# Performance work log

Hardware: AMD Instinct MI355X
Metric: run time of the kernel (lower is better)

The kernel has to match this reference:

```python
import jax, jax.numpy as jnp
import numpy as np

N = 50000
E = 800000
D_IN = 128
D_OUT = 128
LN_EPS = 1e-5
DROP_P = 0.1


def setup_inputs() -> dict:
    key = jax.random.key(0)
    ks = jax.random.split(key, 8)
    x = jax.random.normal(ks[0], (N, D_IN), dtype=jnp.float32)
    edge_index = jax.random.randint(ks[1], (2, E), 0, N, dtype=jnp.int64)
    # dropout mask: binary keep-mask scaled by 1/(1-p), as torch dropout produces
    u = jax.random.uniform(ks[2], (N, D_IN), dtype=jnp.float32)
    dropout_mask = (u > DROP_P).astype(jnp.float32) / (1.0 - DROP_P)
    # LayerNorm affine params
    gamma = jnp.ones((D_IN,), dtype=jnp.float32)
    beta = jnp.zeros((D_IN,), dtype=jnp.float32)
    # SAGEConv linears: lin_l (aggregated neighbors, with bias), lin_r (root, no bias)
    s = 1.0 / np.sqrt(D_IN)
    w_l = jax.random.uniform(ks[3], (D_OUT, D_IN), minval=-s, maxval=s, dtype=jnp.float32)
    b_l = jax.random.uniform(ks[4], (D_OUT,), minval=-s, maxval=s, dtype=jnp.float32)
    w_r = jax.random.uniform(ks[5], (D_OUT, D_IN), minval=-s, maxval=s, dtype=jnp.float32)
    return {"x": x, "edge_index": edge_index, "dropout_mask": dropout_mask,
            "gamma": gamma, "beta": beta, "w_l": w_l, "b_l": b_l, "w_r": w_r}


def reference(x, edge_index, dropout_mask, gamma, beta, w_l, b_l, w_r):
    # LayerNorm + ReLU + dropout mask
    mu = jnp.mean(x, axis=-1, keepdims=True)
    var = jnp.mean(jnp.square(x - mu), axis=-1, keepdims=True)
    h = (x - mu) * jax.lax.rsqrt(var + LN_EPS) * gamma + beta
    h = jax.nn.relu(h) * dropout_mask  # [N, D_IN]
    # SAGEConv: mean-aggregate source features into target nodes
    src = edge_index[0]
    dst = edge_index[1]
    msg = h[src]  # [E, D_IN] gathered messages
    agg = jax.ops.segment_sum(msg, dst, num_segments=N)  # [N, D_IN]
    deg = jax.ops.segment_sum(jnp.ones((E,), dtype=h.dtype), dst, num_segments=N)
    agg = agg / jnp.maximum(deg, 1.0)[:, None]
    # out = lin_l(agg) + lin_r(h)
    out = agg @ w_l.T + b_l + h @ w_r.T  # [N, D_OUT]
    return out
```

## Files before the change

kernel.cpp:

```cpp
#include <hip/hip_runtime.h>
#include <hip/hip_bf16.h>

#define N_NODES 50000
#define N_EDGES 800000
#define D 128
#define NB_SCAN ((N_NODES + 255) / 256)

typedef short bf16x8 __attribute__((ext_vector_type(8)));
typedef float f32x4 __attribute__((ext_vector_type(4)));

__device__ __forceinline__ unsigned int bf16u(float f) {
  __hip_bfloat16 b = __float2bfloat16(f);
  return (unsigned int)*reinterpret_cast<unsigned short*>(&b);
}

__global__ __launch_bounds__(256) void gemm_kernel(
    const float* __restrict__ x, const float* __restrict__ mask,
    const float* __restrict__ gamma, const float* __restrict__ beta,
    const float* __restrict__ w_l, const float* __restrict__ w_r,
    const float* __restrict__ b_l, unsigned int* __restrict__ gb,
    float* __restrict__ rp, int* __restrict__ deg) {
  __shared__ unsigned short Bs[64 * 64 * 8];
  const int t = threadIdx.x;
  const int w = t >> 6;
  const int l = t & 63;
  const int lm = l & 15;
  const int quad = l >> 4;
  const int nb = blockIdx.x * 64;

  if (blockIdx.x < NB_SCAN) {
    const int i = blockIdx.x * 256 + t;
    if (i < N_NODES) deg[i] = 0;
  }

#pragma unroll
  for (int i = 0; i < 16; ++i) {
    const int fid = w * 16 + i;
    const int sub = fid >> 2;
    const int ch = fid & 3;
    const float* srcw = (sub < 8) ? (w_l + (size_t)(sub * 16 + lm) * D)
                                  : (w_r + (size_t)((sub - 8) * 16 + lm) * D);
    const float4 a = *(const float4*)(srcw + ch * 32 + quad * 8);
    const float4 b = *(const float4*)(srcw + ch * 32 + quad * 8 + 4);
    uint4 v;
    v.x = (bf16u(a.y) << 16) | bf16u(a.x);
    v.y = (bf16u(a.w) << 16) | bf16u(a.z);
    v.z = (bf16u(b.y) << 16) | bf16u(b.x);
    v.w = (bf16u(b.w) << 16) | bf16u(b.z);
    *(uint4*)(Bs + ((size_t)fid * 64 + l) * 8) = v;
  }

  int anode = nb + w * 16 + lm;
  if (anode >= N_NODES) anode = N_NODES - 1;
  const float* xrow = x + (size_t)anode * D;
  float xv[32];
  float s = 0.f, q = 0.f;
#pragma unroll
  for (int ch = 0; ch < 4; ++ch) {
    const float4 a = *(const float4*)(xrow + ch * 32 + quad * 8);
    const float4 b = *(const float4*)(xrow + ch * 32 + quad * 8 + 4);
    xv[ch * 8 + 0] = a.x; xv[ch * 8 + 1] = a.y;
    xv[ch * 8 + 2] = a.z; xv[ch * 8 + 3] = a.w;
    xv[ch * 8 + 4] = b.x; xv[ch * 8 + 5] = b.y;
    xv[ch * 8 + 6] = b.z; xv[ch * 8 + 7] = b.w;
    s += (a.x + a.y) + (a.z + a.w) + (b.x + b.y) + (b.z + b.w);
    q += a.x * a.x + a.y * a.y + a.z * a.z + a.w * a.w +
         b.x * b.x + b.y * b.y + b.z * b.z + b.w * b.w;
  }
  s += __shfl_xor(s, 16);
  s += __shfl_xor(s, 32);
  q += __shfl_xor(q, 16);
  q += __shfl_xor(q, 32);
  const float mean = s * (1.0f / 128.0f);
  const float var = q * (1.0f / 128.0f) - mean * mean;
  const float rs = rsqrtf(var + 1e-5f);

  const float* mrow = mask + (size_t)anode * D;
  bf16x8 af[4];
#pragma unroll
  for (int ch = 0; ch < 4; ++ch) {
    const int c0 = ch * 32 + quad * 8;
    const float4 g0 = *(const float4*)(gamma + c0);
    const float4 g1 = *(const float4*)(gamma + c0 + 4);
    const float4 b0 = *(const float4*)(beta + c0);
    const float4 b1 = *(const float4*)(beta + c0 + 4);
    const float4 m0 = *(const float4*)(mrow + c0);
    const float4 m1 = *(const float4*)(mrow + c0 + 4);
    const float gv[8] = {g0.x, g0.y, g0.z, g0.w, g1.x, g1.y, g1.z, g1.w};
    const float bv[8] = {b0.x, b0.y, b0.z, b0.w, b1.x, b1.y, b1.z, b1.w};
    const float mv[8] = {m0.x, m0.y, m0.z, m0.w, m1.x, m1.y, m1.z, m1.w};
#pragma unroll
    for (int j = 0; j < 8; ++j) {
      const float hv =
          fmaxf((xv[ch * 8 + j] - mean) * rs * gv[j] + bv[j], 0.0f) * mv[j];
      af[ch][j] = (short)bf16u(hv);
    }
  }
  __syncthreads();

  f32x4 acc[16];
#pragma unroll
  for (int sub = 0; sub < 16; ++sub) acc[sub] = (f32x4){0.f, 0.f, 0.f, 0.f};
  const bf16x8* BsF = (const bf16x8*)Bs;
#pragma unroll
  for (int sub = 0; sub < 16; ++sub)
#pragma unroll
    for (int ch = 0; ch < 4; ++ch)
      acc[sub] = __builtin_amdgcn_mfma_f32_16x16x32_bf16(
          af[ch], BsF[(sub * 4 + ch) * 64 + l], acc[sub], 0, 0, 0);

  float blv[8];
#pragma unroll
  for (int j = 0; j < 8; ++j) blv[j] = b_l[j * 16 + lm];

  const int node0 = nb + w * 16 + quad * 4;
#pragma unroll
  for (int reg = 0; reg < 4; ++reg) {
    const int node = node0 + reg;
    if (node < N_NODES) {
      uint4 p;
      p.x = (bf16u(acc[1][reg]) << 16) | bf16u(acc[0][reg]);
      p.y = (bf16u(acc[3][reg]) << 16) | bf16u(acc[2][reg]);
      p.z = (bf16u(acc[5][reg]) << 16) | bf16u(acc[4][reg]);
      p.w = (bf16u(acc[7][reg]) << 16) | bf16u(acc[6][reg]);
      ((uint4*)gb)[(size_t)node * 16 + lm] = p;
      float4 q0, q1;
      q0.x = acc[8][reg] + blv[0];
      q0.y = acc[9][reg] + blv[1];
      q0.z = acc[10][reg] + blv[2];
      q0.w = acc[11][reg] + blv[3];
      q1.x = acc[12][reg] + blv[4];
      q1.y = acc[13][reg] + blv[5];
      q1.z = acc[14][reg] + blv[6];
      q1.w = acc[15][reg] + blv[7];
      ((float4*)rp)[(size_t)node * 32 + lm * 2 + 0] = q0;
      ((float4*)rp)[(size_t)node * 32 + lm * 2 + 1] = q1;
    }
  }
}

__global__ __launch_bounds__(256) void hist_kernel(const int* __restrict__ ei,
                                                   int* __restrict__ deg,
                                                   int* __restrict__ rank) {
  const int e = (blockIdx.x * 256 + threadIdx.x) * 4;
  if (e + 3 < N_EDGES) {
    const int4 d4 = *(const int4*)(ei + N_EDGES + e);
    int4 r4;
    r4.x = atomicAdd(&deg[d4.x], 1);
    r4.y = atomicAdd(&deg[d4.y], 1);
    r4.z = atomicAdd(&deg[d4.z], 1);
    r4.w = atomicAdd(&deg[d4.w], 1);
    *(int4*)(rank + e) = r4;
  } else {
    for (int k = e; k < N_EDGES; ++k)
      rank[k] = atomicAdd(&deg[ei[N_EDGES + k]], 1);
  }
}

__global__ __launch_bounds__(256) void scan1_kernel(
    const int* __restrict__ deg, int* __restrict__ offL1,
    int* __restrict__ partial) {
  __shared__ int sm[256];
  const int t = threadIdx.x;
  const int i = blockIdx.x * 256 + t;
  const int v = (i < N_NODES) ? deg[i] : 0;
  sm[t] = v;
  __syncthreads();
#pragma unroll
  for (int ofs = 1; ofs < 256; ofs <<= 1) {
    int x = sm[t];
    if (t >= ofs) x += sm[t - ofs];
    __syncthreads();
    sm[t] = x;
    __syncthreads();
  }
  if (i < N_NODES) offL1[i] = sm[t] - v;
  if (t == 255) partial[blockIdx.x] = sm[255];
}

__global__ __launch_bounds__(256) void scan2_kernel(int* __restrict__ partial) {
  __shared__ int sm[256];
  const int t = threadIdx.x;
  const int v = (t < NB_SCAN) ? partial[t] : 0;
  sm[t] = v;
  __syncthreads();
#pragma unroll
  for (int ofs = 1; ofs < 256; ofs <<= 1) {
    int x = sm[t];
    if (t >= ofs) x += sm[t - ofs];
    __syncthreads();
    sm[t] = x;
    __syncthreads();
  }
  if (t < NB_SCAN) partial[t] = sm[t] - v;
}

__global__ __launch_bounds__(256) void scatter_kernel(
    const int* __restrict__ ei, const int* __restrict__ offL1,
    const int* __restrict__ partial, const int* __restrict__ rank,
    int* __restrict__ csr) {
  const int e = (blockIdx.x * 256 + threadIdx.x) * 4;
  if (e + 3 < N_EDGES) {
    const int4 s4 = *(const int4*)(ei + e);
    const int4 d4 = *(const int4*)(ei + N_EDGES + e);
    const int4 r4 = *(const int4*)(rank + e);
    csr[offL1[d4.x] + partial[d4.x >> 8] + r4.x] = s4.x;
    csr[offL1[d4.y] + partial[d4.y >> 8] + r4.y] = s4.y;
    csr[offL1[d4.z] + partial[d4.z >> 8] + r4.z] = s4.z;
    csr[offL1[d4.w] + partial[d4.w >> 8] + r4.w] = s4.w;
  } else {
    for (int k = e; k < N_EDGES; ++k) {
      const int dst = ei[N_EDGES + k];
      csr[offL1[dst] + partial[dst >> 8] + rank[k]] = ei[k];
    }
  }
}

#define ACC8(v)                                     \
  do {                                              \
    acc[0] += __uint_as_float((v).x << 16);         \
    acc[1] += __uint_as_float((v).x & 0xffff0000u); \
    acc[2] += __uint_as_float((v).y << 16);         \
    acc[3] += __uint_as_float((v).y & 0xffff0000u); \
    acc[4] += __uint_as_float((v).z << 16);         \
    acc[5] += __uint_as_float((v).z & 0xffff0000u); \
    acc[6] += __uint_as_float((v).w << 16);         \
    acc[7] += __uint_as_float((v).w & 0xffff0000u); \
  } while (0)

__global__ __launch_bounds__(256) void agg_kernel(
    const int* __restrict__ offL1, const int* __restrict__ partial,
    const int* __restrict__ csr, const unsigned int* __restrict__ gb,
    const float* __restrict__ rp, float* __restrict__ out) {
  const int l = threadIdx.x & 63;
  const int q = l >> 4;
  const int c = l & 15;
  const int n = blockIdx.x * 4 + (threadIdx.x >> 6);
  const int s = offL1[n] + partial[n >> 8];
  const int e = (n + 1 < N_NODES) ? offL1[n + 1] + partial[(n + 1) >> 8]
                                  : N_EDGES;
  const uint4* g4 = (const uint4*)gb;
  float acc[8];
#pragma unroll
  for (int k = 0; k < 8; ++k) acc[k] = 0.0f;
  for (int base = s; base < e; base += 64) {
    const int cnt = min(e - base, 64);
    int idx = (l < cnt) ? csr[base + l] : 0;
    int j = 0;
    for (; j + 16 <= cnt; j += 16) {
      const int i0 = __shfl(idx, j + 0 + q);
      const int i1 = __shfl(idx, j + 4 + q);
      const int i2 = __shfl(idx, j + 8 + q);
      const int i3 = __shfl(idx, j + 12 + q);
      const uint4 v0 = g4[(size_t)i0 * 16 + c];
      const uint4 v1 = g4[(size_t)i1 * 16 + c];
      const uint4 v2 = g4[(size_t)i2 * 16 + c];
      const uint4 v3 = g4[(size_t)i3 * 16 + c];
      ACC8(v0);
      ACC8(v1);
      ACC8(v2);
      ACC8(v3);
    }
    for (; j + 4 <= cnt; j += 4) {
      const int i0 = __shfl(idx, j + q);
      const uint4 v0 = g4[(size_t)i0 * 16 + c];
      ACC8(v0);
    }
    if (j < cnt) {
      const int rem = cnt - j;
      const int i0 = __shfl(idx, j + min(q, rem - 1));
      if (q < rem) {
        const uint4 v0 = g4[(size_t)i0 * 16 + c];
        ACC8(v0);
      }
    }
  }
#pragma unroll
  for (int k = 0; k < 8; ++k) {
    acc[k] += __shfl_xor(acc[k], 16);
    acc[k] += __shfl_xor(acc[k], 32);
  }
  if (l < 16) {
    const float inv = 1.0f / fmaxf((float)(e - s), 1.0f);
    const float4 rp0 = ((const float4*)rp)[(size_t)n * 32 + c * 2 + 0];
    const float4 rp1 = ((const float4*)rp)[(size_t)n * 32 + c * 2 + 1];
    float* o = out + (size_t)n * D + c;
    o[0]   = fmaf(acc[0], inv, rp0.x);
    o[16]  = fmaf(acc[1], inv, rp0.y);
    o[32]  = fmaf(acc[2], inv, rp0.z);
    o[48]  = fmaf(acc[3], inv, rp0.w);
    o[64]  = fmaf(acc[4], inv, rp1.x);
    o[80]  = fmaf(acc[5], inv, rp1.y);
    o[96]  = fmaf(acc[6], inv, rp1.z);
    o[112] = fmaf(acc[7], inv, rp1.w);
  }
}

extern "C" void kernel_launch(void* const* d_in, const int* in_sizes, int n_in,
                              void* d_out, int out_size, void* d_ws,
                              size_t ws_size, hipStream_t stream) {
  const float* x = (const float*)d_in[0];
  const int* ei = (const int*)d_in[1];
  const float* mask = (const float*)d_in[2];
  const float* gamma = (const float*)d_in[3];
  const float* beta = (const float*)d_in[4];
  const float* w_l = (const float*)d_in[5];
  const float* b_l = (const float*)d_in[6];
  const float* w_r = (const float*)d_in[7];
  float* out = (float*)d_out;

  char* ws = (char*)d_ws;
  size_t off = 0;
  auto alloc = [&](size_t bytes) {
    char* p = ws + off;
    off += (bytes + 255) & ~(size_t)255;
    return p;
  };
  unsigned int* gb =
      (unsigned int*)alloc((size_t)N_NODES * D * sizeof(unsigned short));
  float* rp = (float*)alloc((size_t)N_NODES * D * sizeof(float));
  int* deg = (int*)alloc((size_t)N_NODES * sizeof(int));
  int* offL1 = (int*)alloc((size_t)N_NODES * sizeof(int));
  int* partial = (int*)alloc((size_t)NB_SCAN * sizeof(int));
  int* rank = (int*)alloc((size_t)N_EDGES * sizeof(int));
  int* csr = (int*)alloc((size_t)N_EDGES * sizeof(int));

  gemm_kernel<<<(N_NODES + 63) / 64, 256, 0, stream>>>(
      x, mask, gamma, beta, w_l, w_r, b_l, gb, rp, deg);
  hist_kernel<<<(N_EDGES / 4 + 255) / 256, 256, 0, stream>>>(ei, deg, rank);
  scan1_kernel<<<NB_SCAN, 256, 0, stream>>>(deg, offL1, partial);
  scan2_kernel<<<1, 256, 0, stream>>>(partial);
  scatter_kernel<<<(N_EDGES / 4 + 255) / 256, 256, 0, stream>>>(
      ei, offL1, partial, rank, csr);
  agg_kernel<<<N_NODES / 4, 256, 0, stream>>>(offL1, partial, csr, gb, rp,
                                              out);
}
```

Measured before the change: 220.8 us.

## Fuse degree histogram into GEMM kernel and merge two-level scan via last-block

Moves the per-edge degree histogram and rank atomics into the GEMM kernel, with each of the 782 GEMM blocks covering 1024 edges, so the atomics overlap with the matrix work. A small zero kernel now clears the degree array and a done counter before the GEMM runs. The two scan kernels are merged into one: each block publishes its partial sum with a release store, and the last block to finish, found through an atomic counter, scans the partials into a separate array. This removes two kernel launches in exchange for an extra zero kernel and atomic traffic inside the GEMM, which may add contention or latency there.

```diff
diff --git a/kernel.cpp b/kernel.cpp
--- a/kernel.cpp
+++ b/kernel.cpp
@@ -5,6 +5,8 @@
 #define N_EDGES 800000
 #define D 128
 #define NB_SCAN ((N_NODES + 255) / 256)
+#define NB_GEMM ((N_NODES + 63) / 64)
+#define EDGES_PER_GEMM_BLOCK 1024
 
 typedef short bf16x8 __attribute__((ext_vector_type(8)));
 typedef float f32x4 __attribute__((ext_vector_type(4)));
@@ -12,6 +14,13 @@
 __device__ __forceinline__ unsigned int bf16u(float f) {
   __hip_bfloat16 b = __float2bfloat16(f);
   return (unsigned int)*reinterpret_cast<unsigned short*>(&b);
+}
+
+__global__ __launch_bounds__(256) void zero_kernel(int* __restrict__ deg,
+                                                   int* __restrict__ done) {
+  const int i = blockIdx.x * 256 + threadIdx.x;
+  if (i < N_NODES) deg[i] = 0;
+  if (i == 0) *done = 0;
 }
 
 __global__ __launch_bounds__(256) void gemm_kernel(
@@ -19,7 +28,8 @@
     const float* __restrict__ gamma, const float* __restrict__ beta,
     const float* __restrict__ w_l, const float* __restrict__ w_r,
     const float* __restrict__ b_l, unsigned int* __restrict__ gb,
-    float* __restrict__ rp, int* __restrict__ deg) {
+    float* __restrict__ rp, const int* __restrict__ ei,
+    int* __restrict__ deg, int* __restrict__ rank) {
   __shared__ unsigned short Bs[64 * 64 * 8];
   const int t = threadIdx.x;
   const int w = t >> 6;
@@ -28,9 +38,20 @@
   const int quad = l >> 4;
   const int nb = blockIdx.x * 64;
 
-  if (blockIdx.x < NB_SCAN) {
-    const int i = blockIdx.x * 256 + t;
-    if (i < N_NODES) deg[i] = 0;
+  {
+    const int e = blockIdx.x * EDGES_PER_GEMM_BLOCK + t * 4;
+    if (e + 3 < N_EDGES) {
+      const int4 d4 = *(const int4*)(ei + N_EDGES + e);
+      int4 r4;
+      r4.x = atomicAdd(&deg[d4.x], 1);
+      r4.y = atomicAdd(&deg[d4.y], 1);
+      r4.z = atomicAdd(&deg[d4.z], 1);
+      r4.w = atomicAdd(&deg[d4.w], 1);
+      *(int4*)(rank + e) = r4;
+    } else {
+      for (int k = e; k < N_EDGES; ++k)
+        rank[k] = atomicAdd(&deg[ei[N_EDGES + k]], 1);
+    }
   }
 
 #pragma unroll
@@ -139,28 +160,12 @@
   }
 }
 
-__global__ __launch_bounds__(256) void hist_kernel(const int* __restrict__ ei,
-                                                   int* __restrict__ deg,
-                                                   int* __restrict__ rank) {
-  const int e = (blockIdx.x * 256 + threadIdx.x) * 4;
-  if (e + 3 < N_EDGES) {
-    const int4 d4 = *(const int4*)(ei + N_EDGES + e);
-    int4 r4;
-    r4.x = atomicAdd(&deg[d4.x], 1);
-    r4.y = atomicAdd(&deg[d4.y], 1);
-    r4.z = atomicAdd(&deg[d4.z], 1);
-    r4.w = atomicAdd(&deg[d4.w], 1);
-    *(int4*)(rank + e) = r4;
-  } else {
-    for (int k = e; k < N_EDGES; ++k)
-      rank[k] = atomicAdd(&deg[ei[N_EDGES + k]], 1);
-  }
-}
-
-__global__ __launch_bounds__(256) void scan1_kernel(
+__global__ __launch_bounds__(256) void scan12_kernel(
     const int* __restrict__ deg, int* __restrict__ offL1,
-    int* __restrict__ partial) {
+    int* __restrict__ partial, int* __restrict__ partial2,
+    int* __restrict__ done) {
   __shared__ int sm[256];
+  __shared__ int amLast;
   const int t = threadIdx.x;
   const int i = blockIdx.x * 256 + t;
   const int v = (i < N_NODES) ? deg[i] : 0;
@@ -175,43 +180,48 @@
     __syncthreads();
   }
   if (i < N_NODES) offL1[i] = sm[t] - v;
-  if (t == 255) partial[blockIdx.x] = sm[255];
-}
-
-__global__ __launch_bounds__(256) void scan2_kernel(int* __restrict__ partial) {
-  __shared__ int sm[256];
-  const int t = threadIdx.x;
-  const int v = (t < NB_SCAN) ? partial[t] : 0;
-  sm[t] = v;
+  if (t == 255)
+    __hip_atomic_store(&partial[blockIdx.x], sm[255], __ATOMIC_RELEASE,
+                       __HIP_MEMORY_SCOPE_AGENT);
   __syncthreads();
-#pragma unroll
-  for (int ofs = 1; ofs < 256; ofs <<= 1) {
-    int x = sm[t];
-    if (t >= ofs) x += sm[t - ofs];
+  if (t == 0) amLast = (atomicAdd(done, 1) == gridDim.x - 1);
+  __syncthreads();
+  if (amLast) {
+    const int pv = (t < NB_SCAN)
+                       ? __hip_atomic_load(&partial[t], __ATOMIC_ACQUIRE,
+                                           __HIP_MEMORY_SCOPE_AGENT)
+                       : 0;
+    sm[t] = pv;
     __syncthreads();
-    sm[t] = x;
-    __syncthreads();
-  }
-  if (t < NB_SCAN) partial[t] = sm[t] - v;
+#pragma unroll
+    for (int ofs = 1; ofs < 256; ofs <<= 1) {
+      int x = sm[t];
+      if (t >= ofs) x += sm[t - ofs];
+      __syncthreads();
+      sm[t] = x;
+      __syncthreads();
+    }
+    if (t < NB_SCAN) partial2[t] = sm[t] - pv;
+  }
 }
 
 __global__ __launch_bounds__(256) void scatter_kernel(
     const int* __restrict__ ei, const int* __restrict__ offL1,
-    const int* __restrict__ partial, const int* __restrict__ rank,
+    const int* __restrict__ partial2, const int* __restrict__ rank,
     int* __restrict__ csr) {
   const int e = (blockIdx.x * 256 + threadIdx.x) * 4;
   if (e + 3 < N_EDGES) {
     const int4 s4 = *(const int4*)(ei + e);
     const int4 d4 = *(const int4*)(ei + N_EDGES + e);
     const int4 r4 = *(const int4*)(rank + e);
-    csr[offL1[d4.x] + partial[d4.x >> 8] + r4.x] = s4.x;
-    csr[offL1[d4.y] + partial[d4.y >> 8] + r4.y] = s4.y;
-    csr[offL1[d4.z] + partial[d4.z >> 8] + r4.z] = s4.z;
-    csr[offL1[d4.w] + partial[d4.w >> 8] + r4.w] = s4.w;
+    csr[offL1[d4.x] + partial2[d4.x >> 8] + r4.x] = s4.x;
+    csr[offL1[d4.y] + partial2[d4.y >> 8] + r4.y] = s4.y;
+    csr[offL1[d4.z] + partial2[d4.z >> 8] + r4.z] = s4.z;
+    csr[offL1[d4.w] + partial2[d4.w >> 8] + r4.w] = s4.w;
   } else {
     for (int k = e; k < N_EDGES; ++k) {
       const int dst = ei[N_EDGES + k];
-      csr[offL1[dst] + partial[dst >> 8] + rank[k]] = ei[k];
+      csr[offL1[dst] + partial2[dst >> 8] + rank[k]] = ei[k];
     }
   }
 }
@@ -229,15 +239,15 @@
   } while (0)
 
 __global__ __launch_bounds__(256) void agg_kernel(
-    const int* __restrict__ offL1, const int* __restrict__ partial,
+    const int* __restrict__ offL1, const int* __restrict__ partial2,
     const int* __restrict__ csr, const unsigned int* __restrict__ gb,
     const float* __restrict__ rp, float* __restrict__ out) {
   const int l = threadIdx.x & 63;
   const int q = l >> 4;
   const int c = l & 15;
   const int n = blockIdx.x * 4 + (threadIdx.x >> 6);
-  const int s = offL1[n] + partial[n >> 8];
-  const int e = (n + 1 < N_NODES) ? offL1[n + 1] + partial[(n + 1) >> 8]
+  const int s = offL1[n] + partial2[n >> 8];
+  const int e = (n + 1 < N_NODES) ? offL1[n + 1] + partial2[(n + 1) >> 8]
                                   : N_EDGES;
   const uint4* g4 = (const uint4*)gb;
   float acc[8];
@@ -322,16 +332,18 @@
   int* deg = (int*)alloc((size_t)N_NODES * sizeof(int));
   int* offL1 = (int*)alloc((size_t)N_NODES * sizeof(int));
   int* partial = (int*)alloc((size_t)NB_SCAN * sizeof(int));
+  int* partial2 = (int*)alloc((size_t)NB_SCAN * sizeof(int));
+  int* done = (int*)alloc(sizeof(int));
   int* rank = (int*)alloc((size_t)N_EDGES * sizeof(int));
   int* csr = (int*)alloc((size_t)N_EDGES * sizeof(int));
 
-  gemm_kernel<<<(N_NODES + 63) / 64, 256, 0, stream>>>(
-      x, mask, gamma, beta, w_l, w_r, b_l, gb, rp, deg);
-  hist_kernel<<<(N_EDGES / 4 + 255) / 256, 256, 0, stream>>>(ei, deg, rank);
-  scan1_kernel<<<NB_SCAN, 256, 0, stream>>>(deg, offL1, partial);
-  scan2_kernel<<<1, 256, 0, stream>>>(partial);
+  zero_kernel<<<NB_SCAN, 256, 0, stream>>>(deg, done);
+  gemm_kernel<<<NB_GEMM, 256, 0, stream>>>(x, mask, gamma, beta, w_l, w_r,
+                                           b_l, gb, rp, ei, deg, rank);
+  scan12_kernel<<<NB_SCAN, 256, 0, stream>>>(deg, offL1, partial, partial2,
+                                             done);
   scatter_kernel<<<(N_EDGES / 4 + 255) / 256, 256, 0, stream>>>(
-      ei, offL1, partial, rank, csr);
-  agg_kernel<<<N_NODES / 4, 256, 0, stream>>>(offL1, partial, csr, gb, rp,
+      ei, offL1, partial2, rank, csr);
+  agg_kernel<<<N_NODES / 4, 256, 0, stream>>>(offL1, partial2, csr, gb, rp,
                                               out);
 }
```

New measurement: 208.7 us. 1.06x faster.
